# Kernel tuning notes

Hardware: AMD Instinct MI355X
Metric: run time of the kernel (lower is better)

Reference implementation:

```python
import jax, jax.numpy as jnp
import numpy as np

N_WORDS = 262144
N_TAGS = 512
BDIM = 768
MDIM = 128


def setup_inputs() -> dict:
    key = jax.random.key(0)
    k1, k2, k3, k4, k5, k6 = jax.random.split(key, 6)
    scale = 1.0 / np.sqrt(BDIM)
    return {
        "tags_embed": jax.random.normal(k1, (N_TAGS, BDIM), dtype=jnp.float32),
        "words_embed": jax.random.normal(k2, (N_WORDS, BDIM), dtype=jnp.float32),
        "tags_W": jax.random.normal(k3, (MDIM, BDIM), dtype=jnp.float32) * scale,
        "tags_b": jax.random.normal(k4, (MDIM,), dtype=jnp.float32) * scale,
        "words_W": jax.random.normal(k5, (MDIM, BDIM), dtype=jnp.float32) * scale,
        "words_b": jax.random.normal(k6, (MDIM,), dtype=jnp.float32) * scale,
    }


def reference(tags_embed, words_embed, tags_W, tags_b, words_W, words_b):
    # Linear projections into the metric space: [T, M] and [N, M]
    tags_m = tags_embed @ tags_W.T + tags_b
    words_m = words_embed @ words_W.T + words_b
    # Pairwise squared Euclidean distances via ||w||^2 + ||t||^2 - 2 w.t
    # (same math as the expand-subtract-pow-sum, GEMM-based instead)
    w_sq = jnp.sum(words_m * words_m, axis=1, keepdims=True)  # [N, 1]
    t_sq = jnp.sum(tags_m * tags_m, axis=1)[None, :]          # [1, T]
    distances = w_sq + t_sq - 2.0 * (words_m @ tags_m.T)      # [N, T]
    logits = -distances
    log_pred_y = jax.nn.log_softmax(logits, axis=1)
    pred_y = jax.nn.softmax(logits, axis=1)
    return (log_pred_y, pred_y)
```

## Files before the change

### kernel.cpp

```cpp
#include <hip/hip_runtime.h>

#define N_WORDS 262144
#define N_TAGS  512
#define BDIM    768
#define MDIM    128
#define KS      32
#define NSL     (BDIM / KS)
#define BW      64

typedef __attribute__((ext_vector_type(8))) short  bf16x8;
typedef __attribute__((ext_vector_type(4))) float  f32x4;

#define GLOAD16(ldsdst, gsrc) __builtin_amdgcn_global_load_lds( \
    (const __attribute__((address_space(1))) unsigned int*)(gsrc), \
    (__attribute__((address_space(3))) unsigned int*)(ldsdst), 16, 0, 0)

__device__ inline unsigned bf16_1(float a) {
    union { float f; unsigned u; } ua; ua.f = a;
    unsigned x = ua.u;
    x += 0x7fffu + ((x >> 16) & 1u);
    return x >> 16;
}
__device__ inline unsigned bf16_2(float a, float b) {
    union { float f; unsigned u; } ua, ub; ua.f = a; ub.f = b;
    unsigned x = ua.u, y = ub.u;
    x += 0x7fffu + ((x >> 16) & 1u);
    y += 0x7fffu + ((y >> 16) & 1u);
    return (x >> 16) | (y & 0xffff0000u);
}

__global__ __launch_bounds__(128) void tags_kernel(
    const float* __restrict__ tags_embed, const float* __restrict__ tags_W,
    const float* __restrict__ tags_b, const float* __restrict__ words_b,
    unsigned short* __restrict__ Tbf, float* __restrict__ cvec)
{
    __shared__ __align__(16) float sE[BDIM];
    __shared__ float red[128];
    const int t = blockIdx.x;
    const int m = threadIdx.x;

    for (int i = m; i < BDIM; i += 128) sE[i] = tags_embed[(size_t)t * BDIM + i];
    __syncthreads();

    float acc = tags_b[m];
    const float* Wr = tags_W + (size_t)m * BDIM;
    #pragma unroll 8
    for (int b = 0; b < BDIM; b += 4) {
        float4 w4 = *reinterpret_cast<const float4*>(Wr + b);
        float4 e4 = *reinterpret_cast<const float4*>(&sE[b]);
        acc += w4.x * e4.x + w4.y * e4.y + w4.z * e4.z + w4.w * e4.w;
    }
    Tbf[(size_t)t * MDIM + m] = (unsigned short)bf16_1(2.0f * acc);

    red[m] = acc * (2.0f * words_b[m] - acc);
    __syncthreads();
    for (int s = 64; s > 0; s >>= 1) {
        if (m < s) red[m] += red[m + s];
        __syncthreads();
    }
    if (m == 0) cvec[t] = red[0];
}

__global__ __launch_bounds__(256) void wt_kernel(
    const float* __restrict__ W, unsigned short* __restrict__ Wtbf)
{
    __shared__ float sT[32][33];
    const int bm = blockIdx.x & 3, bk = blockIdx.x >> 2;
    const int m0 = bm * 32, k0 = bk * 32;
    const int r = threadIdx.x >> 3, c = threadIdx.x & 7;

    f32x4 w4 = *reinterpret_cast<const f32x4*>(W + (size_t)(m0 + r) * BDIM + k0 + c * 4);
    sT[r][c * 4 + 0] = w4.x;  sT[r][c * 4 + 1] = w4.y;
    sT[r][c * 4 + 2] = w4.z;  sT[r][c * 4 + 3] = w4.w;
    __syncthreads();

    unsigned lo = bf16_2(sT[c * 4 + 0][r], sT[c * 4 + 1][r]);
    unsigned hi = bf16_2(sT[c * 4 + 2][r], sT[c * 4 + 3][r]);
    unsigned long long p = ((unsigned long long)hi << 32) | lo;
    *reinterpret_cast<unsigned long long*>(Wtbf + (size_t)(k0 + r) * MDIM + m0 + c * 4) = p;
}

__global__ __launch_bounds__(64) void gt_kernel(
    const unsigned short* __restrict__ Wtbf, const unsigned short* __restrict__ Tbf,
    unsigned short* __restrict__ GtSl)
{
    const int kt = blockIdx.x % 48, tg = blockIdx.x / 48;
    const int k0 = kt * 16, t0 = tg * 64;
    const int n = threadIdx.x & 15, q = threadIdx.x >> 4;

    bf16x8 a[4];
    #pragma unroll
    for (int ks = 0; ks < 4; ++ks)
        a[ks] = *reinterpret_cast<const bf16x8*>(
            Wtbf + (size_t)(k0 + n) * MDIM + ks * 32 + q * 8);

    const int s2  = kt >> 1;
    const int off = (kt & 1) * 16 + 4 * q;

    #pragma unroll
    for (int tt = 0; tt < 4; ++tt) {
        f32x4 acc = (f32x4){0.f, 0.f, 0.f, 0.f};
        #pragma unroll
        for (int ks = 0; ks < 4; ++ks) {
            bf16x8 b = *reinterpret_cast<const bf16x8*>(
                Tbf + (size_t)(t0 + tt * 16 + n) * MDIM + ks * 32 + q * 8);
            acc = __builtin_amdgcn_mfma_f32_16x16x32_bf16(a[ks], b, acc, 0, 0, 0);
        }
        unsigned lo = bf16_2(acc.x, acc.y);
        unsigned hi = bf16_2(acc.z, acc.w);
        unsigned long long p = ((unsigned long long)hi << 32) | lo;
        *reinterpret_cast<unsigned long long*>(
            GtSl + (size_t)s2 * (N_TAGS * KS) + (size_t)(t0 + tt * 16 + n) * KS + off) = p;
    }
}

__global__ __launch_bounds__(512, 4) void main_kernel(
    const float* __restrict__ embed,
    const unsigned short* __restrict__ GtSl,
    const float* __restrict__ cvec,
    float* __restrict__ out_logp, float* __restrict__ out_p)
{
    __shared__ __align__(16) unsigned short sG[2 * N_TAGS * KS];
    __shared__ __align__(16) unsigned short sE[2 * BW * KS];
    __shared__ float sMx[8][BW];
    __shared__ float sSm[8][BW];

    const int tid  = threadIdx.x;
    const int lane = tid & 63;
    const int v    = tid >> 6;
    const int n    = lane & 15;
    const int q    = lane >> 4;
    const int we   = tid >> 3;
    const int kp   = tid & 7;
    const int w0   = blockIdx.x * BW;

    const float* eSrc = embed + (size_t)(w0 + we) * BDIM + kp * 4;

    f32x4 eOld;
    {
        f32x4 e0 = *reinterpret_cast<const f32x4*>(eSrc);
        #pragma unroll
        for (int r = 0; r < 4; ++r)
            GLOAD16(sG + (r * 8 + v) * 512,
                    GtSl + (size_t)((r * 8 + v) * 64 + lane) * 8);
        eOld = *reinterpret_cast<const f32x4*>(eSrc + KS);
        unsigned lo = bf16_2(e0.x, e0.y), hi = bf16_2(e0.z, e0.w);
        *reinterpret_cast<unsigned long long*>(sE + we * KS + kp * 4) =
            ((unsigned long long)hi << 32) | lo;
        asm volatile("s_waitcnt vmcnt(1) lgkmcnt(0)\n\ts_barrier" ::: "memory");
    }

    f32x4 acc[4][4];
    #pragma unroll
    for (int mt = 0; mt < 4; ++mt)
        #pragma unroll
        for (int wt = 0; wt < 4; ++wt)
            acc[mt][wt] = (f32x4){0.f, 0.f, 0.f, 0.f};

    int cur = 0;
    for (int s = 0; s < NSL; ++s) {
        const int nxt = cur ^ 1;

        if (s + 1 < NSL) {
            #pragma unroll
            for (int r = 0; r < 4; ++r)
                GLOAD16(sG + nxt * (N_TAGS * KS) + (r * 8 + v) * 512,
                        GtSl + (size_t)(s + 1) * (N_TAGS * KS)
                             + (size_t)((r * 8 + v) * 64 + lane) * 8);
        }
        f32x4 eNew;
        if (s + 2 < NSL)
            eNew = *reinterpret_cast<const f32x4*>(eSrc + (s + 2) * KS);

        if (s + 1 < NSL) {
            unsigned lo = bf16_2(eOld.x, eOld.y), hi = bf16_2(eOld.z, eOld.w);
            *reinterpret_cast<unsigned long long*>(
                sE + nxt * (BW * KS) + we * KS + kp * 4) =
                ((unsigned long long)hi << 32) | lo;
        }

        const unsigned short* sGc = sG + cur * (N_TAGS * KS);
        const unsigned short* sEc = sE + cur * (BW * KS);
        bf16x8 a[4], b[4];
        #pragma unroll
        for (int mt = 0; mt < 4; ++mt)
            a[mt] = *reinterpret_cast<const bf16x8*>(
                sGc + (v * 64 + mt * 16 + n) * KS + q * 8);
        #pragma unroll
        for (int wt = 0; wt < 4; ++wt)
            b[wt] = *reinterpret_cast<const bf16x8*>(
                sEc + (wt * 16 + n) * KS + q * 8);
        #pragma unroll
        for (int mt = 0; mt < 4; ++mt)
            #pragma unroll
            for (int wt = 0; wt < 4; ++wt)
                acc[mt][wt] = __builtin_amdgcn_mfma_f32_16x16x32_bf16(
                    a[mt], b[wt], acc[mt][wt], 0, 0, 0);

        if (s + 2 < NSL) {
            asm volatile("s_waitcnt vmcnt(1) lgkmcnt(0)\n\ts_barrier" ::: "memory");
        } else if (s + 1 < NSL) {
            asm volatile("s_waitcnt vmcnt(0) lgkmcnt(0)\n\ts_barrier" ::: "memory");
        }
        eOld = eNew;
        cur = nxt;
    }

    #pragma unroll
    for (int mt = 0; mt < 4; ++mt) {
        f32x4 c4 = *reinterpret_cast<const f32x4*>(cvec + v * 64 + mt * 16 + 4 * q);
        #pragma unroll
        for (int wt = 0; wt < 4; ++wt) acc[mt][wt] += c4;
    }

    float mx[4], sm[4];
    #pragma unroll
    for (int wt = 0; wt < 4; ++wt) {
        float m = -3.0e38f;
        #pragma unroll
        for (int mt = 0; mt < 4; ++mt)
            m = fmaxf(m, fmaxf(fmaxf(acc[mt][wt].x, acc[mt][wt].y),
                               fmaxf(acc[mt][wt].z, acc[mt][wt].w)));
        m = fmaxf(m, __shfl_xor(m, 16, 64));
        m = fmaxf(m, __shfl_xor(m, 32, 64));
        mx[wt] = m;
        float s = 0.f;
        #pragma unroll
        for (int mt = 0; mt < 4; ++mt)
            s += __expf(acc[mt][wt].x - m) + __expf(acc[mt][wt].y - m)
               + __expf(acc[mt][wt].z - m) + __expf(acc[mt][wt].w - m);
        s += __shfl_xor(s, 16, 64);
        s += __shfl_xor(s, 32, 64);
        sm[wt] = s;
    }
    if (q == 0) {
        #pragma unroll
        for (int wt = 0; wt < 4; ++wt) {
            sMx[v][wt * 16 + n] = mx[wt];
            sSm[v][wt * 16 + n] = sm[wt];
        }
    }
    __syncthreads();

    #pragma unroll
    for (int wt = 0; wt < 4; ++wt) {
        const int wd = wt * 16 + n;
        float M = sMx[0][wd];
        #pragma unroll
        for (int u = 1; u < 8; ++u) M = fmaxf(M, sMx[u][wd]);
        float S = 0.f;
        #pragma unroll
        for (int u = 0; u < 8; ++u) S += sSm[u][wd] * __expf(sMx[u][wd] - M);
        const float neg = M + __logf(S);

        const size_t row = (size_t)(w0 + wd) * N_TAGS + v * 64 + 4 * q;
        #pragma unroll
        for (int mt = 0; mt < 4; ++mt) {
            f32x4 lp, pp;
            lp.x = acc[mt][wt].x - neg;  pp.x = __expf(lp.x);
            lp.y = acc[mt][wt].y - neg;  pp.y = __expf(lp.y);
            lp.z = acc[mt][wt].z - neg;  pp.z = __expf(lp.z);
            lp.w = acc[mt][wt].w - neg;  pp.w = __expf(lp.w);
            *reinterpret_cast<f32x4*>(out_logp + row + mt * 16) = lp;
            *reinterpret_cast<f32x4*>(out_p    + row + mt * 16) = pp;
        }
    }
}

extern "C" void kernel_launch(void* const* d_in, const int* in_sizes, int n_in,
                              void* d_out, int out_size, void* d_ws, size_t ws_size,
                              hipStream_t stream) {
    const float* tags_embed  = (const float*)d_in[0];
    const float* words_embed = (const float*)d_in[1];
    const float* tags_W      = (const float*)d_in[2];
    const float* tags_b      = (const float*)d_in[3];
    const float* words_W     = (const float*)d_in[4];
    const float* words_b     = (const float*)d_in[5];

    float* out_logp = (float*)d_out;
    float* out_p    = out_logp + (size_t)N_WORDS * N_TAGS;

    unsigned short* Tbf  = (unsigned short*)d_ws;
    float*          cvec = (float*)(Tbf + (size_t)N_TAGS * MDIM);
    unsigned short* Wtbf = (unsigned short*)(cvec + N_TAGS);
    unsigned short* GtSl = Wtbf + (size_t)BDIM * MDIM;

    tags_kernel<<<N_TAGS, 128, 0, stream>>>(tags_embed, tags_W, tags_b, words_b, Tbf, cvec);
    wt_kernel<<<96, 256, 0, stream>>>(words_W, Wtbf);
    gt_kernel<<<384, 64, 0, stream>>>(Wtbf, Tbf, GtSl);
    main_kernel<<<N_WORDS / BW, 512, 0, stream>>>(
        words_embed, GtSl, cvec, out_logp, out_p);
}
```

Measured before the change: 575.2 us.

## Load tag-projection operands directly into registers instead of staging through LDS

```diff
diff --git a/kernel.cpp b/kernel.cpp
--- a/kernel.cpp
+++ b/kernel.cpp
@@ -11,10 +11,6 @@
 typedef __attribute__((ext_vector_type(8))) short  bf16x8;
 typedef __attribute__((ext_vector_type(4))) float  f32x4;
 
-#define GLOAD16(ldsdst, gsrc) __builtin_amdgcn_global_load_lds( \
-    (const __attribute__((address_space(1))) unsigned int*)(gsrc), \
-    (__attribute__((address_space(3))) unsigned int*)(ldsdst), 16, 0, 0)
-
 __device__ inline unsigned bf16_1(float a) {
     union { float f; unsigned u; } ua; ua.f = a;
     unsigned x = ua.u;
@@ -120,7 +116,6 @@
     const float* __restrict__ cvec,
     float* __restrict__ out_logp, float* __restrict__ out_p)
 {
-    __shared__ __align__(16) unsigned short sG[2 * N_TAGS * KS];
     __shared__ __align__(16) unsigned short sE[2 * BW * KS];
     __shared__ float sMx[8][BW];
     __shared__ float sSm[8][BW];
@@ -135,19 +130,20 @@
     const int w0   = blockIdx.x * BW;
 
     const float* eSrc = embed + (size_t)(w0 + we) * BDIM + kp * 4;
+    const unsigned short* Ab = GtSl + (size_t)(v * 64 + n) * KS + q * 8;
 
     f32x4 eOld;
+    bf16x8 aC[4], aN[4];
     {
         f32x4 e0 = *reinterpret_cast<const f32x4*>(eSrc);
         #pragma unroll
-        for (int r = 0; r < 4; ++r)
-            GLOAD16(sG + (r * 8 + v) * 512,
-                    GtSl + (size_t)((r * 8 + v) * 64 + lane) * 8);
+        for (int mt = 0; mt < 4; ++mt)
+            aC[mt] = *reinterpret_cast<const bf16x8*>(Ab + mt * (16 * KS));
         eOld = *reinterpret_cast<const f32x4*>(eSrc + KS);
         unsigned lo = bf16_2(e0.x, e0.y), hi = bf16_2(e0.z, e0.w);
         *reinterpret_cast<unsigned long long*>(sE + we * KS + kp * 4) =
             ((unsigned long long)hi << 32) | lo;
-        asm volatile("s_waitcnt vmcnt(1) lgkmcnt(0)\n\ts_barrier" ::: "memory");
+        asm volatile("s_waitcnt lgkmcnt(0)\n\ts_barrier" ::: "memory");
     }
 
     f32x4 acc[4][4];
@@ -161,48 +157,41 @@
     for (int s = 0; s < NSL; ++s) {
         const int nxt = cur ^ 1;
 
+        f32x4 eNew;
         if (s + 1 < NSL) {
             #pragma unroll
-            for (int r = 0; r < 4; ++r)
-                GLOAD16(sG + nxt * (N_TAGS * KS) + (r * 8 + v) * 512,
-                        GtSl + (size_t)(s + 1) * (N_TAGS * KS)
-                             + (size_t)((r * 8 + v) * 64 + lane) * 8);
-        }
-        f32x4 eNew;
-        if (s + 2 < NSL)
-            eNew = *reinterpret_cast<const f32x4*>(eSrc + (s + 2) * KS);
-
-        if (s + 1 < NSL) {
+            for (int mt = 0; mt < 4; ++mt)
+                aN[mt] = *reinterpret_cast<const bf16x8*>(
+                    Ab + (size_t)(s + 1) * (N_TAGS * KS) + mt * (16 * KS));
+            if (s + 2 < NSL)
+                eNew = *reinterpret_cast<const f32x4*>(eSrc + (s + 2) * KS);
             unsigned lo = bf16_2(eOld.x, eOld.y), hi = bf16_2(eOld.z, eOld.w);
             *reinterpret_cast<unsigned long long*>(
                 sE + nxt * (BW * KS) + we * KS + kp * 4) =
                 ((unsigned long long)hi << 32) | lo;
         }
 
-        const unsigned short* sGc = sG + cur * (N_TAGS * KS);
         const unsigned short* sEc = sE + cur * (BW * KS);
-        bf16x8 a[4], b[4];
-        #pragma unroll
-        for (int mt = 0; mt < 4; ++mt)
-            a[mt] = *reinterpret_cast<const bf16x8*>(
-                sGc + (v * 64 + mt * 16 + n) * KS + q * 8);
+        bf16x8 b[4];
         #pragma unroll
         for (int wt = 0; wt < 4; ++wt)
             b[wt] = *reinterpret_cast<const bf16x8*>(
                 sEc + (wt * 16 + n) * KS + q * 8);
+        __builtin_amdgcn_s_setprio(1);
         #pragma unroll
         for (int mt = 0; mt < 4; ++mt)
             #pragma unroll
             for (int wt = 0; wt < 4; ++wt)
                 acc[mt][wt] = __builtin_amdgcn_mfma_f32_16x16x32_bf16(
-                    a[mt], b[wt], acc[mt][wt], 0, 0, 0);
-
-        if (s + 2 < NSL) {
-            asm volatile("s_waitcnt vmcnt(1) lgkmcnt(0)\n\ts_barrier" ::: "memory");
-        } else if (s + 1 < NSL) {
-            asm volatile("s_waitcnt vmcnt(0) lgkmcnt(0)\n\ts_barrier" ::: "memory");
-        }
-        eOld = eNew;
+                    aC[mt], b[wt], acc[mt][wt], 0, 0, 0);
+        __builtin_amdgcn_s_setprio(0);
+
+        if (s + 1 < NSL) {
+            asm volatile("s_waitcnt lgkmcnt(0)\n\ts_barrier" ::: "memory");
+            #pragma unroll
+            for (int mt = 0; mt < 4; ++mt) aC[mt] = aN[mt];
+            eOld = eNew;
+        }
         cur = nxt;
     }
 
```

Result: slower. 615.4 us (+7.0%).

## Make main kernel persistent over panels and overlap output stores with next GEMM

Applied to the files above, without the earlier changes.

```diff
diff --git a/kernel.cpp b/kernel.cpp
--- a/kernel.cpp
+++ b/kernel.cpp
@@ -6,10 +6,12 @@
 #define MDIM    128
 #define KS      32
 #define NSL     (BDIM / KS)
-#define BW      64
+#define BW      32
+#define NPAN    8
 
 typedef __attribute__((ext_vector_type(8))) short  bf16x8;
 typedef __attribute__((ext_vector_type(4))) float  f32x4;
+typedef __attribute__((ext_vector_type(2))) float  f32x2;
 
 #define GLOAD16(ldsdst, gsrc) __builtin_amdgcn_global_load_lds( \
     (const __attribute__((address_space(1))) unsigned int*)(gsrc), \
@@ -27,6 +29,9 @@
     x += 0x7fffu + ((x >> 16) & 1u);
     y += 0x7fffu + ((y >> 16) & 1u);
     return (x >> 16) | (y & 0xffff0000u);
+}
+__device__ inline f32x2 ntld2(const float* p) {
+    return __builtin_nontemporal_load(reinterpret_cast<const f32x2*>(p));
 }
 
 __global__ __launch_bounds__(128) void tags_kernel(
@@ -114,53 +119,84 @@
     }
 }
 
-__global__ __launch_bounds__(512, 4) void main_kernel(
-    const float* __restrict__ embed,
-    const unsigned short* __restrict__ GtSl,
-    const float* __restrict__ cvec,
+__device__ __forceinline__ const float* pro(
+    const float* __restrict__ embed, const unsigned short* __restrict__ GtSl,
+    unsigned short* sG, unsigned short* sE,
+    int v, int lane, int we, int kp, int w0p, f32x2& eOld)
+{
+    const float* eSrc = embed + (size_t)(w0p + we) * BDIM + kp * 2;
+    #pragma unroll
+    for (int r = 0; r < 4; ++r)
+        GLOAD16(sG + (r * 8 + v) * 512,
+                GtSl + (size_t)((r * 8 + v) * 64 + lane) * 8);
+    f32x2 e0 = ntld2(eSrc);
+    eOld = ntld2(eSrc + KS);
+    *reinterpret_cast<unsigned*>(sE + we * KS + kp * 2) = bf16_2(e0.x, e0.y);
+    asm volatile("s_waitcnt vmcnt(1) lgkmcnt(0)\n\ts_barrier" ::: "memory");
+    return eSrc;
+}
+
+template<bool DOST>
+__device__ __forceinline__ void kloop(
+    const float* __restrict__ eSrc, const unsigned short* __restrict__ GtSl,
+    unsigned short* sG, unsigned short* sE,
+    const int v, const int lane, const int n, const int q,
+    const int we, const int kp, f32x2& eOld,
+    f32x4 (&acc)[4][2],
+    const f32x4 (&accP)[4][2], const float (&negP)[2],
+    const unsigned long long (&offP)[2],
     float* __restrict__ out_logp, float* __restrict__ out_p)
 {
-    __shared__ __align__(16) unsigned short sG[2 * N_TAGS * KS];
-    __shared__ __align__(16) unsigned short sE[2 * BW * KS];
-    __shared__ float sMx[8][BW];
-    __shared__ float sSm[8][BW];
-
-    const int tid  = threadIdx.x;
-    const int lane = tid & 63;
-    const int v    = tid >> 6;
-    const int n    = lane & 15;
-    const int q    = lane >> 4;
-    const int we   = tid >> 3;
-    const int kp   = tid & 7;
-    const int w0   = blockIdx.x * BW;
-
-    const float* eSrc = embed + (size_t)(w0 + we) * BDIM + kp * 4;
-
-    f32x4 eOld;
-    {
-        f32x4 e0 = *reinterpret_cast<const f32x4*>(eSrc);
+    #pragma unroll
+    for (int mt = 0; mt < 4; ++mt) {
+        acc[mt][0] = (f32x4){0.f, 0.f, 0.f, 0.f};
+        acc[mt][1] = (f32x4){0.f, 0.f, 0.f, 0.f};
+    }
+
+    #pragma unroll
+    for (int s = 0; s < 8; ++s) {
+        const int nxt = (s & 1) ^ 1;
         #pragma unroll
         for (int r = 0; r < 4; ++r)
-            GLOAD16(sG + (r * 8 + v) * 512,
-                    GtSl + (size_t)((r * 8 + v) * 64 + lane) * 8);
-        eOld = *reinterpret_cast<const f32x4*>(eSrc + KS);
-        unsigned lo = bf16_2(e0.x, e0.y), hi = bf16_2(e0.z, e0.w);
-        *reinterpret_cast<unsigned long long*>(sE + we * KS + kp * 4) =
-            ((unsigned long long)hi << 32) | lo;
-        asm volatile("s_waitcnt vmcnt(1) lgkmcnt(0)\n\ts_barrier" ::: "memory");
-    }
-
-    f32x4 acc[4][4];
-    #pragma unroll
-    for (int mt = 0; mt < 4; ++mt)
-        #pragma unroll
-        for (int wt = 0; wt < 4; ++wt)
-            acc[mt][wt] = (f32x4){0.f, 0.f, 0.f, 0.f};
+            GLOAD16(sG + nxt * (N_TAGS * KS) + (r * 8 + v) * 512,
+                    GtSl + (size_t)(s + 1) * (N_TAGS * KS)
+                         + (size_t)((r * 8 + v) * 64 + lane) * 8);
+        f32x2 eN = ntld2(eSrc + (s + 2) * KS);
+        *reinterpret_cast<unsigned*>(sE + nxt * (BW * KS) + we * KS + kp * 2) =
+            bf16_2(eOld.x, eOld.y);
+        if constexpr (DOST) {
+            const int smt = s >> 1, swt = s & 1;
+            f32x4 d = accP[smt][swt] - negP[swt];
+            *reinterpret_cast<f32x4*>(out_logp + offP[swt] + smt * 16) = d;
+            f32x4 e;
+            e.x = __expf(d.x); e.y = __expf(d.y);
+            e.z = __expf(d.z); e.w = __expf(d.w);
+            *reinterpret_cast<f32x4*>(out_p + offP[swt] + smt * 16) = e;
+        }
+        {
+            const unsigned short* sGc = sG + (s & 1) * (N_TAGS * KS);
+            const unsigned short* sEc = sE + (s & 1) * (BW * KS);
+            bf16x8 b0 = *reinterpret_cast<const bf16x8*>(sEc + n * KS + q * 8);
+            bf16x8 b1 = *reinterpret_cast<const bf16x8*>(sEc + (16 + n) * KS + q * 8);
+            #pragma unroll
+            for (int mt = 0; mt < 4; ++mt) {
+                bf16x8 a = *reinterpret_cast<const bf16x8*>(
+                    sGc + (v * 64 + mt * 16 + n) * KS + q * 8);
+                acc[mt][0] = __builtin_amdgcn_mfma_f32_16x16x32_bf16(a, b0, acc[mt][0], 0, 0, 0);
+                acc[mt][1] = __builtin_amdgcn_mfma_f32_16x16x32_bf16(a, b1, acc[mt][1], 0, 0, 0);
+            }
+        }
+        if constexpr (DOST)
+            asm volatile("s_waitcnt vmcnt(3) lgkmcnt(0)\n\ts_barrier" ::: "memory");
+        else
+            asm volatile("s_waitcnt vmcnt(1) lgkmcnt(0)\n\ts_barrier" ::: "memory");
+        eOld = eN;
+    }
 
     int cur = 0;
-    for (int s = 0; s < NSL; ++s) {
+    #pragma unroll 1
+    for (int s = 8; s < NSL; ++s) {
         const int nxt = cur ^ 1;
-
         if (s + 1 < NSL) {
             #pragma unroll
             for (int r = 0; r < 4; ++r)
@@ -168,54 +204,49 @@
                         GtSl + (size_t)(s + 1) * (N_TAGS * KS)
                              + (size_t)((r * 8 + v) * 64 + lane) * 8);
         }
-        f32x4 eNew;
-        if (s + 2 < NSL)
-            eNew = *reinterpret_cast<const f32x4*>(eSrc + (s + 2) * KS);
-
-        if (s + 1 < NSL) {
-            unsigned lo = bf16_2(eOld.x, eOld.y), hi = bf16_2(eOld.z, eOld.w);
-            *reinterpret_cast<unsigned long long*>(
-                sE + nxt * (BW * KS) + we * KS + kp * 4) =
-                ((unsigned long long)hi << 32) | lo;
-        }
-
-        const unsigned short* sGc = sG + cur * (N_TAGS * KS);
-        const unsigned short* sEc = sE + cur * (BW * KS);
-        bf16x8 a[4], b[4];
-        #pragma unroll
-        for (int mt = 0; mt < 4; ++mt)
-            a[mt] = *reinterpret_cast<const bf16x8*>(
-                sGc + (v * 64 + mt * 16 + n) * KS + q * 8);
-        #pragma unroll
-        for (int wt = 0; wt < 4; ++wt)
-            b[wt] = *reinterpret_cast<const bf16x8*>(
-                sEc + (wt * 16 + n) * KS + q * 8);
-        #pragma unroll
-        for (int mt = 0; mt < 4; ++mt)
+        f32x2 eN;
+        if (s + 2 < NSL) eN = ntld2(eSrc + (s + 2) * KS);
+        if (s + 1 < NSL)
+            *reinterpret_cast<unsigned*>(sE + nxt * (BW * KS) + we * KS + kp * 2) =
+                bf16_2(eOld.x, eOld.y);
+        {
+            const unsigned short* sGc = sG + cur * (N_TAGS * KS);
+            const unsigned short* sEc = sE + cur * (BW * KS);
+            bf16x8 b0 = *reinterpret_cast<const bf16x8*>(sEc + n * KS + q * 8);
+            bf16x8 b1 = *reinterpret_cast<const bf16x8*>(sEc + (16 + n) * KS + q * 8);
             #pragma unroll
-            for (int wt = 0; wt < 4; ++wt)
-                acc[mt][wt] = __builtin_amdgcn_mfma_f32_16x16x32_bf16(
-                    a[mt], b[wt], acc[mt][wt], 0, 0, 0);
-
+            for (int mt = 0; mt < 4; ++mt) {
+                bf16x8 a = *reinterpret_cast<const bf16x8*>(
+                    sGc + (v * 64 + mt * 16 + n) * KS + q * 8);
+                acc[mt][0] = __builtin_amdgcn_mfma_f32_16x16x32_bf16(a, b0, acc[mt][0], 0, 0, 0);
+                acc[mt][1] = __builtin_amdgcn_mfma_f32_16x16x32_bf16(a, b1, acc[mt][1], 0, 0, 0);
+            }
+        }
         if (s + 2 < NSL) {
             asm volatile("s_waitcnt vmcnt(1) lgkmcnt(0)\n\ts_barrier" ::: "memory");
         } else if (s + 1 < NSL) {
             asm volatile("s_waitcnt vmcnt(0) lgkmcnt(0)\n\ts_barrier" ::: "memory");
         }
-        eOld = eNew;
+        eOld = eN;
         cur = nxt;
     }
-
+}
+
+__device__ __forceinline__ void softmax_panel(
+    f32x4 (&acc)[4][2], const float* __restrict__ cvec,
+    float* sMx, float* sSm,
+    const int v, const int n, const int q, const int w0p,
+    float (&neg)[2], unsigned long long (&off)[2])
+{
     #pragma unroll
     for (int mt = 0; mt < 4; ++mt) {
         f32x4 c4 = *reinterpret_cast<const f32x4*>(cvec + v * 64 + mt * 16 + 4 * q);
-        #pragma unroll
-        for (int wt = 0; wt < 4; ++wt) acc[mt][wt] += c4;
-    }
-
-    float mx[4], sm[4];
-    #pragma unroll
-    for (int wt = 0; wt < 4; ++wt) {
+        acc[mt][0] += c4;
+        acc[mt][1] += c4;
+    }
+    float mx[2], sm[2];
+    #pragma unroll
+    for (int wt = 0; wt < 2; ++wt) {
         float m = -3.0e38f;
         #pragma unroll
         for (int mt = 0; mt < 4; ++mt)
@@ -234,37 +265,84 @@
         sm[wt] = s;
     }
     if (q == 0) {
-        #pragma unroll
-        for (int wt = 0; wt < 4; ++wt) {
-            sMx[v][wt * 16 + n] = mx[wt];
-            sSm[v][wt * 16 + n] = sm[wt];
-        }
+        sMx[v * 32 + n]      = mx[0];
+        sMx[v * 32 + 16 + n] = mx[1];
+        sSm[v * 32 + n]      = sm[0];
+        sSm[v * 32 + 16 + n] = sm[1];
     }
     __syncthreads();
-
-    #pragma unroll
-    for (int wt = 0; wt < 4; ++wt) {
+    #pragma unroll
+    for (int wt = 0; wt < 2; ++wt) {
         const int wd = wt * 16 + n;
-        float M = sMx[0][wd];
-        #pragma unroll
-        for (int u = 1; u < 8; ++u) M = fmaxf(M, sMx[u][wd]);
+        float M = sMx[wd];
+        #pragma unroll
+        for (int u = 1; u < 8; ++u) M = fmaxf(M, sMx[u * 32 + wd]);
         float S = 0.f;
         #pragma unroll
-        for (int u = 0; u < 8; ++u) S += sSm[u][wd] * __expf(sMx[u][wd] - M);
-        const float neg = M + __logf(S);
-
-        const size_t row = (size_t)(w0 + wd) * N_TAGS + v * 64 + 4 * q;
-        #pragma unroll
-        for (int mt = 0; mt < 4; ++mt) {
-            f32x4 lp, pp;
-            lp.x = acc[mt][wt].x - neg;  pp.x = __expf(lp.x);
-            lp.y = acc[mt][wt].y - neg;  pp.y = __expf(lp.y);
-            lp.z = acc[mt][wt].z - neg;  pp.z = __expf(lp.z);
-            lp.w = acc[mt][wt].w - neg;  pp.w = __expf(lp.w);
-            *reinterpret_cast<f32x4*>(out_logp + row + mt * 16) = lp;
-            *reinterpret_cast<f32x4*>(out_p    + row + mt * 16) = pp;
-        }
-    }
+        for (int u = 0; u < 8; ++u) S += sSm[u * 32 + wd] * __expf(sMx[u * 32 + wd] - M);
+        neg[wt] = M + __logf(S);
+        off[wt] = (unsigned long long)(w0p + wd) * N_TAGS + v * 64 + 4 * q;
+    }
+}
+
+__global__ __launch_bounds__(512, 4) void main_kernel(
+    const float* __restrict__ embed,
+    const unsigned short* __restrict__ GtSl,
+    const float* __restrict__ cvec,
+    float* __restrict__ out_logp, float* __restrict__ out_p)
+{
+    __shared__ __align__(16) unsigned short sG[2 * N_TAGS * KS];
+    __shared__ __align__(16) unsigned short sE[2 * BW * KS];
+    __shared__ float sMx[8 * 32];
+    __shared__ float sSm[8 * 32];
+
+    const int tid  = threadIdx.x;
+    const int lane = tid & 63;
+    const int v    = tid >> 6;
+    const int n    = lane & 15;
+    const int q    = lane >> 4;
+    const int we   = tid >> 4;
+    const int kp   = tid & 15;
+    const int w0base = blockIdx.x * (BW * NPAN);
+
+    f32x4 accA[4][2], accB[4][2];
+    float negA[2], negB[2] = {0.f, 0.f};
+    unsigned long long offA[2], offB[2] = {0ull, 0ull};
+    f32x2 eOld;
+
+    const float* eSrc = pro(embed, GtSl, sG, sE, v, lane, we, kp, w0base, eOld);
+    kloop<false>(eSrc, GtSl, sG, sE, v, lane, n, q, we, kp, eOld,
+                 accA, accB, negB, offB, out_logp, out_p);
+    softmax_panel(accA, cvec, sMx, sSm, v, n, q, w0base, negA, offA);
+    eSrc = pro(embed, GtSl, sG, sE, v, lane, we, kp, w0base + BW, eOld);
+
+    #pragma unroll 1
+    for (int pp = 0; pp < 3; ++pp) {
+        const int p1 = 2 * pp + 1, p2 = 2 * pp + 2;
+        kloop<true>(eSrc, GtSl, sG, sE, v, lane, n, q, we, kp, eOld,
+                    accB, accA, negA, offA, out_logp, out_p);
+        softmax_panel(accB, cvec, sMx, sSm, v, n, q, w0base + p1 * BW, negB, offB);
+        eSrc = pro(embed, GtSl, sG, sE, v, lane, we, kp, w0base + p2 * BW, eOld);
+        kloop<true>(eSrc, GtSl, sG, sE, v, lane, n, q, we, kp, eOld,
+                    accA, accB, negB, offB, out_logp, out_p);
+        softmax_panel(accA, cvec, sMx, sSm, v, n, q, w0base + p2 * BW, negA, offA);
+        eSrc = pro(embed, GtSl, sG, sE, v, lane, we, kp, w0base + (p2 + 1) * BW, eOld);
+    }
+    kloop<true>(eSrc, GtSl, sG, sE, v, lane, n, q, we, kp, eOld,
+                accB, accA, negA, offA, out_logp, out_p);
+    softmax_panel(accB, cvec, sMx, sSm, v, n, q, w0base + 7 * BW, negB, offB);
+
+    #pragma unroll
+    for (int mt = 0; mt < 4; ++mt)
+        #pragma unroll
+        for (int wt = 0; wt < 2; ++wt) {
+            f32x4 d = accB[mt][wt] - negB[wt];
+            *reinterpret_cast<f32x4*>(out_logp + offB[wt] + mt * 16) = d;
+            f32x4 e;
+            e.x = __expf(d.x); e.y = __expf(d.y);
+            e.z = __expf(d.z); e.w = __expf(d.w);
+            *reinterpret_cast<f32x4*>(out_p + offB[wt] + mt * 16) = e;
+        }
 }
 
 extern "C" void kernel_launch(void* const* d_in, const int* in_sizes, int n_in,
@@ -288,6 +366,6 @@
     tags_kernel<<<N_TAGS, 128, 0, stream>>>(tags_embed, tags_W, tags_b, words_b, Tbf, cvec);
     wt_kernel<<<96, 256, 0, stream>>>(words_W, Wtbf);
     gt_kernel<<<384, 64, 0, stream>>>(Wtbf, Tbf, GtSl);
-    main_kernel<<<N_WORDS / BW, 512, 0, stream>>>(
+    main_kernel<<<N_WORDS / (BW * NPAN), 512, 0, stream>>>(
         words_embed, GtSl, cvec, out_logp, out_p);
 }
```

After: 1.127 ms. 1.96x slower.
